# Optimization experiments

Hardware: AMD Instinct MI355X
Metric: run time of the kernel (lower is better)

The kernel has to match this reference:

```python
import jax, jax.numpy as jnp
import numpy as np

B, H, S, D = 2, 8, 2048, 64
N_HASHES = 6
EPS = 1e-8


def setup_inputs() -> dict:
    key = jax.random.key(0)
    kq, kk, kv, kr = jax.random.split(key, 4)
    Q = jax.random.normal(kq, (B, H, S, D), dtype=jnp.float32)
    K = jax.random.normal(kk, (B, H, S, D), dtype=jnp.float32)
    V = jax.random.normal(kv, (B, H, S, D), dtype=jnp.float32)
    rotations = jax.random.normal(kr, (H, N_HASHES, D), dtype=jnp.float32)
    return {"Q": Q, "K": K, "V": V, "rotations": rotations}


def _buckets(X, rotations, powers):
    # X: [b,h,l,d] -> integer bucket id per position, [b,h,l]
    Xn = X / (jnp.linalg.norm(X, axis=-1, keepdims=True) + 1e-8)
    bits = jnp.einsum('bhld,hnd->bhln', Xn, rotations) > 0
    return jnp.sum(bits.astype(jnp.int32) * powers, axis=-1)


def reference(Q, K, V, rotations):
    n_hashes = rotations.shape[1]
    d = Q.shape[-1]
    powers = (2 ** jnp.arange(n_hashes)).astype(jnp.int32)
    q_buckets = _buckets(Q, rotations, powers)  # [b,h,sq]
    k_buckets = _buckets(K, rotations, powers)  # [b,h,sk]
    # queries only attend to keys whose full hash code matches exactly
    match = q_buckets[..., :, None] == k_buckets[..., None, :]  # [b,h,sq,sk]
    scores = jnp.einsum('bhqd,bhkd->bhqk', Q, K) / (d ** 0.5)
    row_has = jnp.any(match, axis=-1, keepdims=True)
    masked = jnp.where(match, scores, -jnp.inf)
    m = jnp.max(masked, axis=-1, keepdims=True)
    m = jnp.where(row_has, m, 0.0)  # avoid -inf for empty rows
    e = jnp.where(match, jnp.exp(scores - m), 0.0)
    weights = e / (jnp.sum(e, axis=-1, keepdims=True) + EPS)
    out = jnp.einsum('bhqk,bhkd->bhqd', weights, V)
    return out / n_hashes
```

## Files before the change

kernel.cpp:

```cpp
#include <hip/hip_runtime.h>
#include <math.h>


constexpr int S_LEN = 2048;
constexpr int D = 64;
constexpr int NHASH = 6;
constexpr int BH = 16;
constexpr int NB = 64;
constexpr int QPAD = 8;
constexpr int PADQ = S_LEN + (QPAD - 1) * NB;

__global__ __launch_bounds__(256) void lsh_buckets2(const float* __restrict__ Q,
                                                    const float* __restrict__ K,
                                                    const float* __restrict__ rot,
                                                    int* __restrict__ qb,
                                                    int* __restrict__ kb) {
    const int gw   = (blockIdx.x * 256 + threadIdx.x) >> 6;
    const int lane = threadIdx.x & 63;
    const bool isK = gw >= BH * S_LEN;
    const int wid  = isK ? gw - BH * S_LEN : gw;
    const float* X = isK ? K : Q;
    int* dst       = isK ? kb : qb;
    const int h    = (wid >> 11) & 7;

    const float x  = X[(size_t)wid * D + lane];
    const float* r = rot + (size_t)h * NHASH * D + lane;
    float p0 = x * r[0 * D], p1 = x * r[1 * D], p2 = x * r[2 * D];
    float p3 = x * r[3 * D], p4 = x * r[4 * D], p5 = x * r[5 * D];
#pragma unroll
    for (int off = 32; off >= 1; off >>= 1) {
        p0 += __shfl_xor(p0, off, 64);
        p1 += __shfl_xor(p1, off, 64);
        p2 += __shfl_xor(p2, off, 64);
        p3 += __shfl_xor(p3, off, 64);
        p4 += __shfl_xor(p4, off, 64);
        p5 += __shfl_xor(p5, off, 64);
    }
    int bucket = (p0 > 0.f ? 1 : 0) | (p1 > 0.f ? 2 : 0) | (p2 > 0.f ? 4 : 0) |
                 (p3 > 0.f ? 8 : 0) | (p4 > 0.f ? 16 : 0) | (p5 > 0.f ? 32 : 0);
    if (lane == 0) dst[wid] = bucket;
}

__global__ __launch_bounds__(256) void lsh_build_lists3(const int* __restrict__ qbuckets,
                                                        const int* __restrict__ kbuckets,
                                                        int* __restrict__ q_plist,
                                                        int* __restrict__ k_start,
                                                        int* __restrict__ k_list) {
    __shared__ unsigned short hist[256][NB + 1];
    __shared__ int base[NB + 1];
    const int which = blockIdx.x >> 4;
    const int bh    = blockIdx.x & 15;
    const int tid   = threadIdx.x;
    const int* src  = (which ? kbuckets : qbuckets) + bh * S_LEN;
    int* blist      = which ? (k_list + bh * S_LEN) : (q_plist + bh * PADQ);

    if (!which) {
        for (int t = tid; t < PADQ; t += 256) blist[t] = -1;
    }

    for (int b = 0; b <= NB; ++b) hist[tid][b] = 0;

    int myb[8];
#pragma unroll
    for (int i = 0; i < 8; ++i) {
        int b = src[tid * 8 + i];
        myb[i] = b;
        hist[tid][b]++;
    }
    __syncthreads();

    if (tid < NB) {
        int run = 0;
        for (int c = 0; c < 256; ++c) {
            int t = hist[c][tid];
            hist[c][tid] = (unsigned short)run;
            run += t;
        }
        base[tid] = run;
    }
    __syncthreads();

    if (tid == 0) {
        int run = 0;
        if (which) {
            int* bstart = k_start + bh * (NB + 1);
            for (int b = 0; b < NB; ++b) {
                int t = base[b];
                base[b] = run;
                bstart[b] = run;
                run += t;
            }
            base[NB] = run;
            bstart[NB] = run;
        } else {
            for (int b = 0; b < NB; ++b) {
                int t = base[b];
                base[b] = run;
                run += (t + QPAD - 1) & ~(QPAD - 1);
            }
        }
    }
    __syncthreads();

#pragma unroll
    for (int i = 0; i < 8; ++i) {
        int b   = myb[i];
        int ofs = base[b] + hist[tid][b];
        hist[tid][b]++;
        blist[ofs] = tid * 8 + i;
    }
}

__global__ __launch_bounds__(256) void lsh_attn_g8(const float* __restrict__ Q,
                                                   const float* __restrict__ K,
                                                   const float* __restrict__ V,
                                                   const int* __restrict__ q_buckets,
                                                   const int* __restrict__ q_plist,
                                                   const int* __restrict__ k_start,
                                                   const int* __restrict__ k_list,
                                                   float* __restrict__ out) {
    __shared__ float wbuf[4][QPAD][64];
    __shared__ int   kbuf[4][64];

    const int wv   = threadIdx.x >> 6;
    const int lane = threadIdx.x & 63;
    const int bh   = blockIdx.y;
    const int slot = (blockIdx.x * 4 + wv) * QPAD;

    const int* pl = q_plist + bh * PADQ + slot;
    int q[QPAD];
    bool vq[QPAD];
    q[0] = __builtin_amdgcn_readfirstlane(pl[0]);
    if (q[0] < 0) return;
#pragma unroll
    for (int j = 1; j < QPAD; ++j) {
        q[j] = __builtin_amdgcn_readfirstlane(pl[j]);
        vq[j] = q[j] >= 0;
        if (!vq[j]) q[j] = q[0];
    }

    const int bucket = __builtin_amdgcn_readfirstlane(q_buckets[bh * S_LEN + q[0]]);
    const int ks = k_start[bh * (NB + 1) + bucket];
    const int ke = k_start[bh * (NB + 1) + bucket + 1];
    const int nk = ke - ks;

    float* outb = out + (size_t)bh * S_LEN * D;
    if (nk == 0) {
        outb[(size_t)q[0] * D + lane] = 0.0f;
#pragma unroll
        for (int j = 1; j < QPAD; ++j)
            if (vq[j]) outb[(size_t)q[j] * D + lane] = 0.0f;
        return;
    }

    const int* kl   = k_list + bh * S_LEN + ks;
    const float* Kb = K + (size_t)bh * S_LEN * D;
    const float* Vb = V + (size_t)bh * S_LEN * D;
    const float* qr[QPAD];
#pragma unroll
    for (int j = 0; j < QPAD; ++j) qr[j] = Q + ((size_t)bh * S_LEN + q[j]) * D;

    float l[QPAD], acc[QPAD];
#pragma unroll
    for (int j = 0; j < QPAD; ++j) { l[j] = 0.f; acc[j] = 0.f; }

    for (int c = 0; c * 64 < nk; ++c) {
        const int cnk  = min(64, nk - c * 64);
        const int kidx = kl[c * 64 + min(lane, cnk - 1)];
        const float* krow = Kb + (size_t)kidx * D;

        float s[QPAD];
#pragma unroll
        for (int j = 0; j < QPAD; ++j) s[j] = 0.f;
#pragma unroll
        for (int d4 = 0; d4 < 16; ++d4) {
            const float4 kv = *(const float4*)(krow + d4 * 4);
#pragma unroll
            for (int j = 0; j < QPAD; ++j) {
                const float4 qv = *(const float4*)(qr[j] + d4 * 4);
                s[j] += qv.x * kv.x + qv.y * kv.y + qv.z * kv.z + qv.w * kv.w;
            }
        }

        const bool kvalid = lane < cnk;
#pragma unroll
        for (int j = 0; j < QPAD; ++j) {
            const float e = kvalid ? __expf(s[j] * 0.125f) : 0.f;
            l[j] += e;
            wbuf[wv][j][lane] = e;
        }
        kbuf[wv][lane] = kidx;

        const int ng = (cnk + 3) >> 2;
        for (int g = 0; g < ng; ++g) {
            const int4 kk = *(const int4*)&kbuf[wv][g * 4];
            const float vx = Vb[(size_t)kk.x * D + lane];
            const float vy = Vb[(size_t)kk.y * D + lane];
            const float vz = Vb[(size_t)kk.z * D + lane];
            const float vw = Vb[(size_t)kk.w * D + lane];
#pragma unroll
            for (int j = 0; j < QPAD; ++j) {
                const float4 e4 = *(const float4*)&wbuf[wv][j][g * 4];
                acc[j] += e4.x * vx + e4.y * vy + e4.z * vz + e4.w * vw;
            }
        }
    }

    float lr[QPAD];
#pragma unroll
    for (int j = 0; j < QPAD; ++j) lr[j] = l[j];
#pragma unroll
    for (int off = 32; off >= 1; off >>= 1) {
#pragma unroll
        for (int j = 0; j < QPAD; ++j) lr[j] += __shfl_xor(lr[j], off, 64);
    }

    const float inv6 = 1.0f / 6.0f;
    outb[(size_t)q[0] * D + lane] = acc[0] / (lr[0] + 1e-8f) * inv6;
#pragma unroll
    for (int j = 1; j < QPAD; ++j)
        if (vq[j]) outb[(size_t)q[j] * D + lane] = acc[j] / (lr[j] + 1e-8f) * inv6;
}

extern "C" void kernel_launch(void* const* d_in, const int* in_sizes, int n_in,
                              void* d_out, int out_size, void* d_ws, size_t ws_size,
                              hipStream_t stream) {
    const float* Q   = (const float*)d_in[0];
    const float* K   = (const float*)d_in[1];
    const float* V   = (const float*)d_in[2];
    const float* rot = (const float*)d_in[3];
    float* out = (float*)d_out;

    char* ws = (char*)d_ws;
    int* q_buckets = (int*)(ws);
    int* k_buckets = (int*)(ws + 131072);
    int* k_start   = (int*)(ws + 262144);
    int* k_list    = (int*)(ws + 270336);
    int* q_plist   = (int*)(ws + 401408);

    lsh_buckets2<<<2 * BH * S_LEN / 4, 256, 0, stream>>>(Q, K, rot, q_buckets, k_buckets);
    lsh_build_lists3<<<32, 256, 0, stream>>>(q_buckets, k_buckets, q_plist, k_start, k_list);
    lsh_attn_g8<<<dim3(PADQ / QPAD / 4, BH), 256, 0, stream>>>(Q, K, V, q_buckets, q_plist,
                                                               k_start, k_list, out);
}
```

Baseline: 88.24 us.

## Split QK dot across half-waves with 4-query groups, Q staged in LDS

```diff
diff --git a/kernel.cpp b/kernel.cpp
--- a/kernel.cpp
+++ b/kernel.cpp
@@ -7,8 +7,9 @@
 constexpr int NHASH = 6;
 constexpr int BH = 16;
 constexpr int NB = 64;
-constexpr int QPAD = 8;
+constexpr int QPAD = 4;
 constexpr int PADQ = S_LEN + (QPAD - 1) * NB;
+constexpr int KCH = 32;
 
 __global__ __launch_bounds__(256) void lsh_buckets2(const float* __restrict__ Q,
                                                     const float* __restrict__ K,
@@ -41,7 +42,7 @@
     if (lane == 0) dst[wid] = bucket;
 }
 
-__global__ __launch_bounds__(256) void lsh_build_lists3(const int* __restrict__ qbuckets,
+__global__ __launch_bounds__(256) void lsh_build_lists4(const int* __restrict__ qbuckets,
                                                         const int* __restrict__ kbuckets,
                                                         int* __restrict__ q_plist,
                                                         int* __restrict__ k_start,
@@ -107,39 +108,45 @@
         int b   = myb[i];
         int ofs = base[b] + hist[tid][b];
         hist[tid][b]++;
-        blist[ofs] = tid * 8 + i;
-    }
-}
-
-__global__ __launch_bounds__(256) void lsh_attn_g8(const float* __restrict__ Q,
-                                                   const float* __restrict__ K,
-                                                   const float* __restrict__ V,
-                                                   const int* __restrict__ q_buckets,
-                                                   const int* __restrict__ q_plist,
-                                                   const int* __restrict__ k_start,
-                                                   const int* __restrict__ k_list,
-                                                   float* __restrict__ out) {
-    __shared__ float wbuf[4][QPAD][64];
-    __shared__ int   kbuf[4][64];
+        int val = tid * 8 + i;
+        if (!which) val |= (b << 16);
+        blist[ofs] = val;
+    }
+}
+
+__global__ __launch_bounds__(256) void lsh_attn_h32(const float* __restrict__ Q,
+                                                    const float* __restrict__ K,
+                                                    const float* __restrict__ V,
+                                                    const int* __restrict__ q_plist,
+                                                    const int* __restrict__ k_start,
+                                                    const int* __restrict__ k_list,
+                                                    float* __restrict__ out) {
+    __shared__ float qlds[4][QPAD][64];
+    __shared__ float wbuf[4][QPAD][KCH];
+    __shared__ int   kbuf[4][KCH];
 
     const int wv   = threadIdx.x >> 6;
     const int lane = threadIdx.x & 63;
+    const int h    = lane >> 5;
+    const int kk   = lane & 31;
     const int bh   = blockIdx.y;
     const int slot = (blockIdx.x * 4 + wv) * QPAD;
 
     const int* pl = q_plist + bh * PADQ + slot;
+    const int e0 = __builtin_amdgcn_readfirstlane(pl[0]);
+    if (e0 < 0) return;
+    const int bucket = e0 >> 16;
+
     int q[QPAD];
     bool vq[QPAD];
-    q[0] = __builtin_amdgcn_readfirstlane(pl[0]);
-    if (q[0] < 0) return;
+    q[0] = e0 & 0xFFFF;
 #pragma unroll
     for (int j = 1; j < QPAD; ++j) {
-        q[j] = __builtin_amdgcn_readfirstlane(pl[j]);
-        vq[j] = q[j] >= 0;
-        if (!vq[j]) q[j] = q[0];
-    }
-
-    const int bucket = __builtin_amdgcn_readfirstlane(q_buckets[bh * S_LEN + q[0]]);
+        const int ej = __builtin_amdgcn_readfirstlane(pl[j]);
+        vq[j] = ej >= 0;
+        q[j] = vq[j] ? (ej & 0xFFFF) : q[0];
+    }
+
     const int ks = k_start[bh * (NB + 1) + bucket];
     const int ke = k_start[bh * (NB + 1) + bucket + 1];
     const int nk = ke - ks;
@@ -156,70 +163,83 @@
     const int* kl   = k_list + bh * S_LEN + ks;
     const float* Kb = K + (size_t)bh * S_LEN * D;
     const float* Vb = V + (size_t)bh * S_LEN * D;
-    const float* qr[QPAD];
-#pragma unroll
-    for (int j = 0; j < QPAD; ++j) qr[j] = Q + ((size_t)bh * S_LEN + q[j]) * D;
-
-    float l[QPAD], acc[QPAD];
-#pragma unroll
-    for (int j = 0; j < QPAD; ++j) { l[j] = 0.f; acc[j] = 0.f; }
-
-    for (int c = 0; c * 64 < nk; ++c) {
-        const int cnk  = min(64, nk - c * 64);
-        const int kidx = kl[c * 64 + min(lane, cnk - 1)];
-        const float* krow = Kb + (size_t)kidx * D;
-
-        float s[QPAD];
-#pragma unroll
-        for (int j = 0; j < QPAD; ++j) s[j] = 0.f;
-#pragma unroll
-        for (int d4 = 0; d4 < 16; ++d4) {
-            const float4 kv = *(const float4*)(krow + d4 * 4);
-#pragma unroll
-            for (int j = 0; j < QPAD; ++j) {
-                const float4 qv = *(const float4*)(qr[j] + d4 * 4);
-                s[j] += qv.x * kv.x + qv.y * kv.y + qv.z * kv.z + qv.w * kv.w;
-            }
-        }
-
-        const bool kvalid = lane < cnk;
-#pragma unroll
-        for (int j = 0; j < QPAD; ++j) {
-            const float e = kvalid ? __expf(s[j] * 0.125f) : 0.f;
-            l[j] += e;
-            wbuf[wv][j][lane] = e;
-        }
-        kbuf[wv][lane] = kidx;
+
+#pragma unroll
+    for (int j = 0; j < QPAD; ++j)
+        qlds[wv][j][lane] = Q[((size_t)bh * S_LEN + q[j]) * D + lane];
+
+    float l0 = 0.f, l1 = 0.f;
+    float acc[QPAD] = {0.f, 0.f, 0.f, 0.f};
+
+    for (int c = 0; c * KCH < nk; ++c) {
+        const int cnk  = min(KCH, nk - c * KCH);
+        const int kidx = kl[c * KCH + min(kk, cnk - 1)];
+        const float* krow = Kb + (size_t)kidx * D + h * 32;
+
+        float s0 = 0.f, s1 = 0.f, s2 = 0.f, s3 = 0.f;
+#pragma unroll
+        for (int i = 0; i < 8; ++i) {
+            const float4 kv = *(const float4*)(krow + i * 4);
+            const float4 qa = *(const float4*)&qlds[wv][0][h * 32 + i * 4];
+            const float4 qb = *(const float4*)&qlds[wv][1][h * 32 + i * 4];
+            const float4 qc = *(const float4*)&qlds[wv][2][h * 32 + i * 4];
+            const float4 qd = *(const float4*)&qlds[wv][3][h * 32 + i * 4];
+            s0 += qa.x * kv.x + qa.y * kv.y + qa.z * kv.z + qa.w * kv.w;
+            s1 += qb.x * kv.x + qb.y * kv.y + qb.z * kv.z + qb.w * kv.w;
+            s2 += qc.x * kv.x + qc.y * kv.y + qc.z * kv.z + qc.w * kv.w;
+            s3 += qd.x * kv.x + qd.y * kv.y + qd.z * kv.z + qd.w * kv.w;
+        }
+        s0 += __shfl_xor(s0, 32, 64);
+        s1 += __shfl_xor(s1, 32, 64);
+        s2 += __shfl_xor(s2, 32, 64);
+        s3 += __shfl_xor(s3, 32, 64);
+
+        const bool kvalid = kk < cnk;
+        const float sa = h ? s2 : s0;
+        const float sb = h ? s3 : s1;
+        const float ea = kvalid ? __expf(sa * 0.125f) : 0.f;
+        const float eb = kvalid ? __expf(sb * 0.125f) : 0.f;
+        l0 += ea;
+        l1 += eb;
+        wbuf[wv][2 * h + 0][kk] = ea;
+        wbuf[wv][2 * h + 1][kk] = eb;
+        if (h == 0) kbuf[wv][kk] = kidx;
 
         const int ng = (cnk + 3) >> 2;
         for (int g = 0; g < ng; ++g) {
-            const int4 kk = *(const int4*)&kbuf[wv][g * 4];
-            const float vx = Vb[(size_t)kk.x * D + lane];
-            const float vy = Vb[(size_t)kk.y * D + lane];
-            const float vz = Vb[(size_t)kk.z * D + lane];
-            const float vw = Vb[(size_t)kk.w * D + lane];
-#pragma unroll
-            for (int j = 0; j < QPAD; ++j) {
-                const float4 e4 = *(const float4*)&wbuf[wv][j][g * 4];
-                acc[j] += e4.x * vx + e4.y * vy + e4.z * vz + e4.w * vw;
-            }
-        }
-    }
-
-    float lr[QPAD];
-#pragma unroll
-    for (int j = 0; j < QPAD; ++j) lr[j] = l[j];
-#pragma unroll
-    for (int off = 32; off >= 1; off >>= 1) {
-#pragma unroll
-        for (int j = 0; j < QPAD; ++j) lr[j] += __shfl_xor(lr[j], off, 64);
-    }
+            const int4 kx = *(const int4*)&kbuf[wv][g * 4];
+            const float vx = Vb[(size_t)kx.x * D + lane];
+            const float vy = Vb[(size_t)kx.y * D + lane];
+            const float vz = Vb[(size_t)kx.z * D + lane];
+            const float vw = Vb[(size_t)kx.w * D + lane];
+            const float4 eA = *(const float4*)&wbuf[wv][0][g * 4];
+            const float4 eB = *(const float4*)&wbuf[wv][1][g * 4];
+            const float4 eC = *(const float4*)&wbuf[wv][2][g * 4];
+            const float4 eD = *(const float4*)&wbuf[wv][3][g * 4];
+            acc[0] += eA.x * vx + eA.y * vy + eA.z * vz + eA.w * vw;
+            acc[1] += eB.x * vx + eB.y * vy + eB.z * vz + eB.w * vw;
+            acc[2] += eC.x * vx + eC.y * vy + eC.z * vz + eC.w * vw;
+            acc[3] += eD.x * vx + eD.y * vy + eD.z * vz + eD.w * vw;
+        }
+    }
+
+#pragma unroll
+    for (int off = 16; off >= 1; off >>= 1) {
+        l0 += __shfl_xor(l0, off, 64);
+        l1 += __shfl_xor(l1, off, 64);
+    }
+    const float o0 = __shfl_xor(l0, 32, 64);
+    const float o1 = __shfl_xor(l1, 32, 64);
+    const float lq0 = h ? o0 : l0;
+    const float lq1 = h ? o1 : l1;
+    const float lq2 = h ? l0 : o0;
+    const float lq3 = h ? l1 : o1;
 
     const float inv6 = 1.0f / 6.0f;
-    outb[(size_t)q[0] * D + lane] = acc[0] / (lr[0] + 1e-8f) * inv6;
-#pragma unroll
-    for (int j = 1; j < QPAD; ++j)
-        if (vq[j]) outb[(size_t)q[j] * D + lane] = acc[j] / (lr[j] + 1e-8f) * inv6;
+    outb[(size_t)q[0] * D + lane] = acc[0] / (lq0 + 1e-8f) * inv6;
+    if (vq[1]) outb[(size_t)q[1] * D + lane] = acc[1] / (lq1 + 1e-8f) * inv6;
+    if (vq[2]) outb[(size_t)q[2] * D + lane] = acc[2] / (lq2 + 1e-8f) * inv6;
+    if (vq[3]) outb[(size_t)q[3] * D + lane] = acc[3] / (lq3 + 1e-8f) * inv6;
 }
 
 extern "C" void kernel_launch(void* const* d_in, const int* in_sizes, int n_in,
@@ -239,7 +259,7 @@
     int* q_plist   = (int*)(ws + 401408);
 
     lsh_buckets2<<<2 * BH * S_LEN / 4, 256, 0, stream>>>(Q, K, rot, q_buckets, k_buckets);
-    lsh_build_lists3<<<32, 256, 0, stream>>>(q_buckets, k_buckets, q_plist, k_start, k_list);
-    lsh_attn_g8<<<dim3(PADQ / QPAD / 4, BH), 256, 0, stream>>>(Q, K, V, q_buckets, q_plist,
-                                                               k_start, k_list, out);
-}
+    lsh_build_lists4<<<32, 256, 0, stream>>>(q_buckets, k_buckets, q_plist, k_start, k_list);
+    lsh_attn_h32<<<dim3(PADQ / QPAD / 4, BH), 256, 0, stream>>>(Q, K, V, q_plist,
+                                                                k_start, k_list, out);
+}
```

Measured after the change: 75.19 us. 14.8% less time.
